# Performance work log

Measured on AMD Instinct MI355X. Metric: run time of the kernel, lower is better.

## Reference

```python
import jax, jax.numpy as jnp
import numpy as np

N_NODES = 50000
HIDDEN = 64
N_EDGES = 800000
HOPS = (1, 2, 3)


def setup_inputs() -> dict:
    key = jax.random.key(0)
    ks = jax.random.split(key, 16)
    d = HIDDEN
    inp = {
        "x": jax.random.normal(ks[0], (N_NODES, d), dtype=jnp.float32),
        "edge_index": jax.random.randint(ks[1], (2, N_EDGES), 0, N_NODES, dtype=jnp.int64),
    }
    s = 1.0 / np.sqrt(d)
    # per-hop GIN MLP params: Linear(d,d) -> ReLU -> Linear(d,d)
    for i in range(len(HOPS)):
        inp[f"W1_{i}"] = jax.random.uniform(ks[2 + 4 * i], (d, d), jnp.float32, -s, s)
        inp[f"b1_{i}"] = jax.random.uniform(ks[3 + 4 * i], (d,), jnp.float32, -s, s)
        inp[f"W2_{i}"] = jax.random.uniform(ks[4 + 4 * i], (d, d), jnp.float32, -s, s)
        inp[f"b2_{i}"] = jax.random.uniform(ks[5 + 4 * i], (d,), jnp.float32, -s, s)
    so = 1.0 / np.sqrt(d * len(HOPS))
    inp["Wo"] = jax.random.uniform(ks[14], (d * len(HOPS), d), jnp.float32, -so, so)
    inp["bo"] = jax.random.uniform(ks[15], (d,), jnp.float32, -so, so)
    return inp


def _gin_conv(h, src, dst, W1, b1, W2, b2):
    # GINConv with eps=0: MLP(x + sum_{j in N(i)} x_j)
    agg = jax.ops.segment_sum(h[src], dst, num_segments=N_NODES)  # [N, d]
    z = h + agg
    z = jax.nn.relu(z @ W1 + b1) @ W2 + b2
    return z


def reference(x, edge_index,
              W1_0, b1_0, W2_0, b2_0,
              W1_1, b1_1, W2_1, b2_1,
              W1_2, b1_2, W2_2, b2_2,
              Wo, bo):
    src, dst = edge_index[0], edge_index[1]
    params = [(W1_0, b1_0, W2_0, b2_0),
              (W1_1, b1_1, W2_1, b2_1),
              (W1_2, b1_2, W2_2, b2_2)]
    outs = []
    for hop, (W1, b1, W2, b2) in zip(HOPS, params):
        h = x
        for _ in range(hop):
            h = _gin_conv(h, src, dst, W1, b1, W2, b2)
        outs.append(h)
    return jnp.concatenate(outs, axis=-1) @ Wo + bo
```

## Files before the change

### kernel.cpp

```cpp
#include <hip/hip_runtime.h>

#define NN 50000
#define NE 800000
#define D  64
#define TILE 64
#define TPB 512
#define NBLK 196


__global__ __launch_bounds__(256) void k_count(const int* __restrict__ ei, int* __restrict__ deg) {
    int e = blockIdx.x * 256 + threadIdx.x;
    if (e < NE) atomicAdd(&deg[ei[NE + e]], 1);
}

__global__ __launch_bounds__(256) void k_bsum(const int* __restrict__ deg, int* __restrict__ bsum) {
    __shared__ int s[256];
    int t = threadIdx.x;
    int i = blockIdx.x * 256 + t;
    s[t] = (i < NN) ? deg[i] : 0;
    __syncthreads();
    for (int off = 128; off > 0; off >>= 1) {
        if (t < off) s[t] += s[t + off];
        __syncthreads();
    }
    if (t == 0) bsum[blockIdx.x] = s[0];
}

__global__ __launch_bounds__(256) void k_scan2(const int* __restrict__ deg,
                                               const int* __restrict__ bsum,
                                               int* __restrict__ row_ptr,
                                               int* __restrict__ cursor) {
    __shared__ int s[256];
    __shared__ int sboff;
    int t = threadIdx.x;
    int b = blockIdx.x;

    int pacc = 0;
    for (int i = t; i < b; i += 256) pacc += bsum[i];
    s[t] = pacc;
    __syncthreads();
    for (int off = 128; off > 0; off >>= 1) {
        if (t < off) s[t] += s[t + off];
        __syncthreads();
    }
    if (t == 0) sboff = s[0];
    __syncthreads();
    int boffv = sboff;
    __syncthreads();

    int i = b * 256 + t;
    int v = (i < NN) ? deg[i] : 0;
    s[t] = v;
    __syncthreads();
    for (int off = 1; off < 256; off <<= 1) {
        int u = (t >= off) ? s[t - off] : 0;
        __syncthreads();
        s[t] += u;
        __syncthreads();
    }
    int excl = s[t] - v + boffv;
    if (i < NN) { row_ptr[i] = excl; cursor[i] = excl; }
    if (b == 0 && t == 0) row_ptr[NN] = NE;
}

__global__ __launch_bounds__(256) void k_fill(const int* __restrict__ ei,
                                              int* __restrict__ cursor,
                                              int* __restrict__ colv) {
    int e = blockIdx.x * 256 + threadIdx.x;
    if (e < NE) {
        int d = ei[NE + e];
        int p = atomicAdd(&cursor[d], 1);
        colv[p] = ei[e];
    }
}


__device__ __forceinline__ float4 gather_row(const float4* __restrict__ h4,
                                             const int* __restrict__ row_ptr,
                                             const int* __restrict__ colv,
                                             int n, int g, int q) {
    float4 a0 = make_float4(0.f, 0.f, 0.f, 0.f);
    float4 a1 = make_float4(0.f, 0.f, 0.f, 0.f);
    float4 a2 = make_float4(0.f, 0.f, 0.f, 0.f);
    float4 a3 = make_float4(0.f, 0.f, 0.f, 0.f);
    if (n >= 0) {
        if (g == 0) a0 = h4[n * 16 + q];
        int e1 = row_ptr[n + 1];
        int e  = row_ptr[n] + g;
        for (; e + 12 < e1; e += 16) {
            int s0 = colv[e], s1 = colv[e + 4], s2 = colv[e + 8], s3 = colv[e + 12];
            float4 v0 = h4[s0 * 16 + q];
            float4 v1 = h4[s1 * 16 + q];
            float4 v2 = h4[s2 * 16 + q];
            float4 v3 = h4[s3 * 16 + q];
            a0.x += v0.x; a0.y += v0.y; a0.z += v0.z; a0.w += v0.w;
            a1.x += v1.x; a1.y += v1.y; a1.z += v1.z; a1.w += v1.w;
            a2.x += v2.x; a2.y += v2.y; a2.z += v2.z; a2.w += v2.w;
            a3.x += v3.x; a3.y += v3.y; a3.z += v3.z; a3.w += v3.w;
        }
        for (; e < e1; e += 4) {
            float4 v = h4[colv[e] * 16 + q];
            a1.x += v.x; a1.y += v.y; a1.z += v.z; a1.w += v.w;
        }
        a0.x += a1.x + a2.x + a3.x;
        a0.y += a1.y + a2.y + a3.y;
        a0.z += a1.z + a2.z + a3.z;
        a0.w += a1.w + a2.w + a3.w;
    }
    a0.x += __shfl_xor(a0.x, 16); a0.y += __shfl_xor(a0.y, 16);
    a0.z += __shfl_xor(a0.z, 16); a0.w += __shfl_xor(a0.w, 16);
    a0.x += __shfl_xor(a0.x, 32); a0.y += __shfl_xor(a0.y, 32);
    a0.z += __shfl_xor(a0.z, 32); a0.w += __shfl_xor(a0.w, 32);
    return a0;
}


__device__ __forceinline__ void conv_body(
    const float4* __restrict__ h4,
    const int* __restrict__ row_ptr,
    const int* __restrict__ colv,
    const float* __restrict__ W1, const float* __restrict__ b1,
    const float* __restrict__ W2, const float* __restrict__ b2,
    float4* __restrict__ out4,
    float (&sW)[D][D], float4 (&sZ4)[TILE][17], float* sB1, float* sB2,
    int node0)
{
    int tid = threadIdx.x;

    {
        const float4* w14 = (const float4*)W1;
        float4* s14 = (float4*)sW;
        for (int i = tid; i < D * D / 4; i += TPB) s14[i] = w14[i];
        if (tid < D) { sB1[tid] = b1[tid]; sB2[tid] = b2[tid]; }
    }

    int wave = tid >> 6, lane = tid & 63;
    int g = lane >> 4, q = lane & 15;

    for (int r = wave; r < TILE; r += (TPB / 64)) {
        int n = node0 + r;
        float4 a = gather_row(h4, row_ptr, colv, (n < NN) ? n : -1, g, q);
        if (g == 0) sZ4[r][q] = a;
    }
    __syncthreads();

    int tr = tid >> 4, tc = tid & 15;
    float* zr0 = (float*)&sZ4[tr * 2 + 0][0];
    float* zr1 = (float*)&sZ4[tr * 2 + 1][0];

    float acc[2][4];
    #pragma unroll
    for (int c = 0; c < 4; ++c) { acc[0][c] = sB1[tc * 4 + c]; acc[1][c] = sB1[tc * 4 + c]; }
    #pragma unroll 16
    for (int k = 0; k < D; ++k) {
        float z0 = zr0[k], z1 = zr1[k];
        #pragma unroll
        for (int c = 0; c < 4; ++c) {
            float w = sW[k][tc * 4 + c];
            acc[0][c] += z0 * w;
            acc[1][c] += z1 * w;
        }
    }
    {
        float4 h0, h1;
        h0.x = fmaxf(acc[0][0], 0.f); h0.y = fmaxf(acc[0][1], 0.f);
        h0.z = fmaxf(acc[0][2], 0.f); h0.w = fmaxf(acc[0][3], 0.f);
        h1.x = fmaxf(acc[1][0], 0.f); h1.y = fmaxf(acc[1][1], 0.f);
        h1.z = fmaxf(acc[1][2], 0.f); h1.w = fmaxf(acc[1][3], 0.f);
        *(float4*)&zr0[tc * 4] = h0;
        *(float4*)&zr1[tc * 4] = h1;
    }
    __syncthreads();

    {
        const float4* w24 = (const float4*)W2;
        float4* s24 = (float4*)sW;
        for (int i = tid; i < D * D / 4; i += TPB) s24[i] = w24[i];
    }
    __syncthreads();

    #pragma unroll
    for (int c = 0; c < 4; ++c) { acc[0][c] = sB2[tc * 4 + c]; acc[1][c] = sB2[tc * 4 + c]; }
    #pragma unroll 16
    for (int k = 0; k < D; ++k) {
        float z0 = zr0[k], z1 = zr1[k];
        #pragma unroll
        for (int c = 0; c < 4; ++c) {
            float w = sW[k][tc * 4 + c];
            acc[0][c] += z0 * w;
            acc[1][c] += z1 * w;
        }
    }
    #pragma unroll
    for (int i = 0; i < 2; ++i) {
        int n = node0 + tr * 2 + i;
        if (n < NN) {
            float4 o;
            o.x = acc[i][0]; o.y = acc[i][1]; o.z = acc[i][2]; o.w = acc[i][3];
            out4[n * 16 + tc] = o;
        }
    }
}

__global__ __launch_bounds__(TPB, 8) void k_conv(
    const float4* __restrict__ h4,
    const int* __restrict__ row_ptr,
    const int* __restrict__ colv,
    const float* __restrict__ W1, const float* __restrict__ b1,
    const float* __restrict__ W2, const float* __restrict__ b2,
    float4* __restrict__ out4)
{
    __shared__ float sW[D][D];
    __shared__ float4 sZ4[TILE][17];
    __shared__ float sB1[D], sB2[D];
    conv_body(h4, row_ptr, colv, W1, b1, W2, b2, out4,
              sW, sZ4, sB1, sB2, blockIdx.x * TILE);
}

__global__ __launch_bounds__(TPB, 8) void k_conv_dual(
    const float4* __restrict__ hA4, const float4* __restrict__ hB4,
    const int* __restrict__ row_ptr,
    const int* __restrict__ colv,
    const float* __restrict__ W1a, const float* __restrict__ b1a,
    const float* __restrict__ W2a, const float* __restrict__ b2a,
    const float* __restrict__ W1b, const float* __restrict__ b1b,
    const float* __restrict__ W2b, const float* __restrict__ b2b,
    float4* __restrict__ outA4, float4* __restrict__ outB4, int nb)
{
    __shared__ float sW[D][D];
    __shared__ float4 sZ4[TILE][17];
    __shared__ float sB1[D], sB2[D];
    int b = blockIdx.x;
    if (b < nb) {
        conv_body(hA4, row_ptr, colv, W1a, b1a, W2a, b2a, outA4,
                  sW, sZ4, sB1, sB2, b * TILE);
    } else {
        conv_body(hB4, row_ptr, colv, W1b, b1b, W2b, b2b, outB4,
                  sW, sZ4, sB1, sB2, (b - nb) * TILE);
    }
}


__global__ __launch_bounds__(TPB) void k_aggmlp3(
    const float4* __restrict__ h4,
    const int* __restrict__ row_ptr,
    const int* __restrict__ colv,
    const float* __restrict__ W1a, const float* __restrict__ b1a,
    const float* __restrict__ W2a, const float* __restrict__ b2a,
    const float* __restrict__ W1b, const float* __restrict__ b1b,
    const float* __restrict__ W2b, const float* __restrict__ b2b,
    const float* __restrict__ W1c, const float* __restrict__ b1c,
    const float* __restrict__ W2c, const float* __restrict__ b2c,
    float4* __restrict__ outA, float4* __restrict__ outB, float4* __restrict__ outC)
{
    __shared__ float sW[D][D];
    __shared__ float4 sZ4[TILE][17];
    __shared__ float4 sH4[TILE][17];
    __shared__ float sB[D];

    int tid = threadIdx.x;
    int node0 = blockIdx.x * TILE;

    int wave = tid >> 6, lane = tid & 63;
    int g = lane >> 4, q = lane & 15;

    for (int r = wave; r < TILE; r += (TPB / 64)) {
        int n = node0 + r;
        float4 a = gather_row(h4, row_ptr, colv, (n < NN) ? n : -1, g, q);
        if (g == 0) sZ4[r][q] = a;
    }

    int tr = tid >> 4, tc = tid & 15;
    float* zr0 = (float*)&sZ4[tr * 2 + 0][0];
    float* zr1 = (float*)&sZ4[tr * 2 + 1][0];
    float* hr0 = (float*)&sH4[tr * 2 + 0][0];
    float* hr1 = (float*)&sH4[tr * 2 + 1][0];

    #pragma unroll 1
    for (int m = 0; m < 3; ++m) {
        const float* W1 = (m == 0) ? W1a : (m == 1) ? W1b : W1c;
        const float* B1 = (m == 0) ? b1a : (m == 1) ? b1b : b1c;
        const float* W2 = (m == 0) ? W2a : (m == 1) ? W2b : W2c;
        const float* B2 = (m == 0) ? b2a : (m == 1) ? b2b : b2c;
        float4* out4 = (m == 0) ? outA : (m == 1) ? outB : outC;

        {
            const float4* w4 = (const float4*)W1;
            float4* s4 = (float4*)sW;
            for (int i = tid; i < D * D / 4; i += TPB) s4[i] = w4[i];
            if (tid < D) sB[tid] = B1[tid];
        }
        __syncthreads();

        float acc[2][4];
        #pragma unroll
        for (int c = 0; c < 4; ++c) { acc[0][c] = sB[tc * 4 + c]; acc[1][c] = sB[tc * 4 + c]; }
        #pragma unroll 16
        for (int k = 0; k < D; ++k) {
            float z0 = zr0[k], z1 = zr1[k];
            #pragma unroll
            for (int c = 0; c < 4; ++c) {
                float w = sW[k][tc * 4 + c];
                acc[0][c] += z0 * w;
                acc[1][c] += z1 * w;
            }
        }
        {
            float4 h0, h1;
            h0.x = fmaxf(acc[0][0], 0.f); h0.y = fmaxf(acc[0][1], 0.f);
            h0.z = fmaxf(acc[0][2], 0.f); h0.w = fmaxf(acc[0][3], 0.f);
            h1.x = fmaxf(acc[1][0], 0.f); h1.y = fmaxf(acc[1][1], 0.f);
            h1.z = fmaxf(acc[1][2], 0.f); h1.w = fmaxf(acc[1][3], 0.f);
            *(float4*)&hr0[tc * 4] = h0;
            *(float4*)&hr1[tc * 4] = h1;
        }
        __syncthreads();

        {
            const float4* w4 = (const float4*)W2;
            float4* s4 = (float4*)sW;
            for (int i = tid; i < D * D / 4; i += TPB) s4[i] = w4[i];
            if (tid < D) sB[tid] = B2[tid];
        }
        __syncthreads();

        #pragma unroll
        for (int c = 0; c < 4; ++c) { acc[0][c] = sB[tc * 4 + c]; acc[1][c] = sB[tc * 4 + c]; }
        #pragma unroll 16
        for (int k = 0; k < D; ++k) {
            float h0 = hr0[k], h1 = hr1[k];
            #pragma unroll
            for (int c = 0; c < 4; ++c) {
                float w = sW[k][tc * 4 + c];
                acc[0][c] += h0 * w;
                acc[1][c] += h1 * w;
            }
        }
        #pragma unroll
        for (int i = 0; i < 2; ++i) {
            int n = node0 + tr * 2 + i;
            if (n < NN) {
                float4 o;
                o.x = acc[i][0]; o.y = acc[i][1]; o.z = acc[i][2]; o.w = acc[i][3];
                out4[n * 16 + tc] = o;
            }
        }
        __syncthreads();
    }
}


__global__ __launch_bounds__(TPB, 8) void k_final(
    const float4* __restrict__ H0, const float4* __restrict__ H1,
    const float4* __restrict__ H2,
    const float* __restrict__ Wo, const float* __restrict__ bo,
    float4* __restrict__ out4)
{
    __shared__ float sW[D][D];
    __shared__ float4 sY4[TILE][17];
    __shared__ float sB[D];

    int tid = threadIdx.x;
    int node0 = blockIdx.x * TILE;
    int tr = tid >> 4, tc = tid & 15;
    const float* yr0 = (const float*)&sY4[tr * 2 + 0][0];
    const float* yr1 = (const float*)&sY4[tr * 2 + 1][0];

    float accO[2][4];

    #pragma unroll 1
    for (int m = 0; m < 3; ++m) {
        const float4* Hc = (m == 0) ? H0 : (m == 1) ? H1 : H2;
        {
            const float4* w4 = (const float4*)(Wo + m * 64 * D);
            float4* s4 = (float4*)sW;
            for (int i = tid; i < D * D / 4; i += TPB) s4[i] = w4[i];
            if (m == 0 && tid < D) sB[tid] = bo[tid];
        }
        for (int i = tid; i < TILE * 16; i += TPB) {
            int r = i >> 4, qq = i & 15;
            int n = node0 + r;
            sY4[r][qq] = (n < NN) ? Hc[n * 16 + qq] : make_float4(0.f, 0.f, 0.f, 0.f);
        }
        __syncthreads();

        if (m == 0) {
            #pragma unroll
            for (int c = 0; c < 4; ++c) { accO[0][c] = sB[tc * 4 + c]; accO[1][c] = sB[tc * 4 + c]; }
        }
        #pragma unroll 16
        for (int k = 0; k < D; ++k) {
            float z0 = yr0[k], z1 = yr1[k];
            #pragma unroll
            for (int c = 0; c < 4; ++c) {
                float w = sW[k][tc * 4 + c];
                accO[0][c] += z0 * w;
                accO[1][c] += z1 * w;
            }
        }
        __syncthreads();
    }

    #pragma unroll
    for (int i = 0; i < 2; ++i) {
        int n = node0 + tr * 2 + i;
        if (n < NN) {
            float4 o;
            o.x = accO[i][0]; o.y = accO[i][1]; o.z = accO[i][2]; o.w = accO[i][3];
            out4[n * 16 + tc] = o;
        }
    }
}


extern "C" void kernel_launch(void* const* d_in, const int* in_sizes, int n_in,
                              void* d_out, int out_size, void* d_ws, size_t ws_size,
                              hipStream_t stream) {
    const float* x    = (const float*)d_in[0];
    const int*   ei   = (const int*)d_in[1];
    const float* W1_0 = (const float*)d_in[2];
    const float* b1_0 = (const float*)d_in[3];
    const float* W2_0 = (const float*)d_in[4];
    const float* b2_0 = (const float*)d_in[5];
    const float* W1_1 = (const float*)d_in[6];
    const float* b1_1 = (const float*)d_in[7];
    const float* W2_1 = (const float*)d_in[8];
    const float* b2_1 = (const float*)d_in[9];
    const float* W1_2 = (const float*)d_in[10];
    const float* b1_2 = (const float*)d_in[11];
    const float* W2_2 = (const float*)d_in[12];
    const float* b2_2 = (const float*)d_in[13];
    const float* Wo   = (const float*)d_in[14];
    const float* bo   = (const float*)d_in[15];
    float4* out = (float4*)d_out;

    char* ws = (char*)d_ws;
    int* deg     = (int*)(ws + 0);
    int* cursor  = (int*)(ws + 200704);
    int* row_ptr = (int*)(ws + 401408);
    int* colv    = (int*)(ws + 602112);
    int* bsum    = (int*)(ws + 3802112);
    float* fbase = (float*)(ws + 3804160);
    float4* H0  = (float4*)(fbase);
    float4* H1  = (float4*)(fbase + 3200000);
    float4* tB  = (float4*)(fbase + 6400000);
    float4* tC2 = (float4*)(fbase + 9600000);
    const float4* x4 = (const float4*)x;

    hipMemsetAsync(deg, 0, NN * sizeof(int), stream);
    k_count<<<(NE + 255) / 256, 256, 0, stream>>>(ei, deg);
    k_bsum <<<NBLK, 256, 0, stream>>>(deg, bsum);
    k_scan2<<<NBLK, 256, 0, stream>>>(deg, bsum, row_ptr, cursor);
    k_fill <<<(NE + 255) / 256, 256, 0, stream>>>(ei, cursor, colv);

    int nb = (NN + TILE - 1) / TILE;

    k_aggmlp3<<<nb, TPB, 0, stream>>>(x4, row_ptr, colv,
                                      W1_0, b1_0, W2_0, b2_0,
                                      W1_1, b1_1, W2_1, b2_1,
                                      W1_2, b1_2, W2_2, b2_2,
                                      H0, tB, out);

    k_conv_dual<<<2 * nb, TPB, 0, stream>>>(
        (const float4*)tB, (const float4*)out, row_ptr, colv,
        W1_1, b1_1, W2_1, b2_1,
        W1_2, b1_2, W2_2, b2_2,
        H1, tC2, nb);

    k_conv<<<nb, TPB, 0, stream>>>((const float4*)tC2, row_ptr, colv,
                                   W1_2, b1_2, W2_2, b2_2, tB);

    k_final<<<nb, TPB, 0, stream>>>((const float4*)H0, (const float4*)H1, (const float4*)tB,
                                    Wo, bo, out);
}
```

Before: 342.6 us.

## Fuse last GIN conv with output projection and drop block-sum scan kernel

```diff
diff --git a/kernel.cpp b/kernel.cpp
--- a/kernel.cpp
+++ b/kernel.cpp
@@ -13,21 +13,7 @@
     if (e < NE) atomicAdd(&deg[ei[NE + e]], 1);
 }
 
-__global__ __launch_bounds__(256) void k_bsum(const int* __restrict__ deg, int* __restrict__ bsum) {
-    __shared__ int s[256];
-    int t = threadIdx.x;
-    int i = blockIdx.x * 256 + t;
-    s[t] = (i < NN) ? deg[i] : 0;
-    __syncthreads();
-    for (int off = 128; off > 0; off >>= 1) {
-        if (t < off) s[t] += s[t + off];
-        __syncthreads();
-    }
-    if (t == 0) bsum[blockIdx.x] = s[0];
-}
-
 __global__ __launch_bounds__(256) void k_scan2(const int* __restrict__ deg,
-                                               const int* __restrict__ bsum,
                                                int* __restrict__ row_ptr,
                                                int* __restrict__ cursor) {
     __shared__ int s[256];
@@ -35,8 +21,9 @@
     int t = threadIdx.x;
     int b = blockIdx.x;
 
+    int lim = b * 256;
     int pacc = 0;
-    for (int i = t; i < b; i += 256) pacc += bsum[i];
+    for (int i = t; i < lim; i += 256) pacc += deg[i];
     s[t] = pacc;
     __syncthreads();
     for (int off = 128; off > 0; off >>= 1) {
@@ -48,7 +35,7 @@
     int boffv = sboff;
     __syncthreads();
 
-    int i = b * 256 + t;
+    int i = lim + t;
     int v = (i < NN) ? deg[i] : 0;
     s[t] = v;
     __syncthreads();
@@ -202,21 +189,6 @@
     }
 }
 
-__global__ __launch_bounds__(TPB, 8) void k_conv(
-    const float4* __restrict__ h4,
-    const int* __restrict__ row_ptr,
-    const int* __restrict__ colv,
-    const float* __restrict__ W1, const float* __restrict__ b1,
-    const float* __restrict__ W2, const float* __restrict__ b2,
-    float4* __restrict__ out4)
-{
-    __shared__ float sW[D][D];
-    __shared__ float4 sZ4[TILE][17];
-    __shared__ float sB1[D], sB2[D];
-    conv_body(h4, row_ptr, colv, W1, b1, W2, b2, out4,
-              sW, sZ4, sB1, sB2, blockIdx.x * TILE);
-}
-
 __global__ __launch_bounds__(TPB, 8) void k_conv_dual(
     const float4* __restrict__ hA4, const float4* __restrict__ hB4,
     const int* __restrict__ row_ptr,
@@ -241,6 +213,161 @@
 }
 
 
+__global__ __launch_bounds__(TPB, 8) void k_conv_last(
+    const float4* __restrict__ h4,
+    const float4* __restrict__ H0, const float4* __restrict__ H1,
+    const int* __restrict__ row_ptr, const int* __restrict__ colv,
+    const float* __restrict__ W1, const float* __restrict__ b1,
+    const float* __restrict__ W2, const float* __restrict__ b2,
+    const float* __restrict__ Wo, const float* __restrict__ bo,
+    float4* __restrict__ out4)
+{
+    __shared__ float sW[D][D];
+    __shared__ float4 sZ4[TILE][17];
+    __shared__ float sB1[D], sB2[D];
+
+    int tid = threadIdx.x;
+    int node0 = blockIdx.x * TILE;
+
+    {
+        const float4* w14 = (const float4*)W1;
+        float4* s14 = (float4*)sW;
+        for (int i = tid; i < D * D / 4; i += TPB) s14[i] = w14[i];
+        if (tid < D) { sB1[tid] = b1[tid]; sB2[tid] = b2[tid]; }
+    }
+
+    int wave = tid >> 6, lane = tid & 63;
+    int g = lane >> 4, q = lane & 15;
+
+    for (int r = wave; r < TILE; r += (TPB / 64)) {
+        int n = node0 + r;
+        float4 a = gather_row(h4, row_ptr, colv, (n < NN) ? n : -1, g, q);
+        if (g == 0) sZ4[r][q] = a;
+    }
+    __syncthreads();
+
+    int tr = tid >> 4, tc = tid & 15;
+    float* zr0 = (float*)&sZ4[tr * 2 + 0][0];
+    float* zr1 = (float*)&sZ4[tr * 2 + 1][0];
+
+    float acc[2][4];
+    #pragma unroll
+    for (int c = 0; c < 4; ++c) { acc[0][c] = sB1[tc * 4 + c]; acc[1][c] = sB1[tc * 4 + c]; }
+    #pragma unroll 16
+    for (int k = 0; k < D; ++k) {
+        float z0 = zr0[k], z1 = zr1[k];
+        #pragma unroll
+        for (int c = 0; c < 4; ++c) {
+            float w = sW[k][tc * 4 + c];
+            acc[0][c] += z0 * w;
+            acc[1][c] += z1 * w;
+        }
+    }
+    {
+        float4 h0, h1;
+        h0.x = fmaxf(acc[0][0], 0.f); h0.y = fmaxf(acc[0][1], 0.f);
+        h0.z = fmaxf(acc[0][2], 0.f); h0.w = fmaxf(acc[0][3], 0.f);
+        h1.x = fmaxf(acc[1][0], 0.f); h1.y = fmaxf(acc[1][1], 0.f);
+        h1.z = fmaxf(acc[1][2], 0.f); h1.w = fmaxf(acc[1][3], 0.f);
+        *(float4*)&zr0[tc * 4] = h0;
+        *(float4*)&zr1[tc * 4] = h1;
+    }
+    __syncthreads();
+
+    {
+        const float4* w24 = (const float4*)W2;
+        float4* s24 = (float4*)sW;
+        for (int i = tid; i < D * D / 4; i += TPB) s24[i] = w24[i];
+    }
+    __syncthreads();
+
+    #pragma unroll
+    for (int c = 0; c < 4; ++c) { acc[0][c] = sB2[tc * 4 + c]; acc[1][c] = sB2[tc * 4 + c]; }
+    #pragma unroll 16
+    for (int k = 0; k < D; ++k) {
+        float z0 = zr0[k], z1 = zr1[k];
+        #pragma unroll
+        for (int c = 0; c < 4; ++c) {
+            float w = sW[k][tc * 4 + c];
+            acc[0][c] += z0 * w;
+            acc[1][c] += z1 * w;
+        }
+    }
+    {
+        float4 h0, h1;
+        h0.x = acc[0][0]; h0.y = acc[0][1]; h0.z = acc[0][2]; h0.w = acc[0][3];
+        h1.x = acc[1][0]; h1.y = acc[1][1]; h1.z = acc[1][2]; h1.w = acc[1][3];
+        *(float4*)&zr0[tc * 4] = h0;
+        *(float4*)&zr1[tc * 4] = h1;
+    }
+    __syncthreads();
+
+    float accO[2][4];
+    int n0 = node0 + tr * 2 + 0;
+    int n1 = node0 + tr * 2 + 1;
+
+    #pragma unroll 1
+    for (int m = 0; m < 3; ++m) {
+        {
+            const float4* w4 = (const float4*)(Wo + m * 64 * D);
+            float4* s4 = (float4*)sW;
+            for (int i = tid; i < D * D / 4; i += TPB) s4[i] = w4[i];
+        }
+        __syncthreads();
+
+        if (m == 0) {
+            #pragma unroll
+            for (int c = 0; c < 4; ++c) { accO[0][c] = sB1[0] * 0.f; }
+            #pragma unroll
+            for (int c = 0; c < 4; ++c) { accO[0][c] = bo[tc * 4 + c]; accO[1][c] = accO[0][c]; }
+        }
+
+        if (m < 2) {
+            const float4* Hc = (m == 0) ? H0 : H1;
+            #pragma unroll 4
+            for (int k4 = 0; k4 < 16; ++k4) {
+                float4 z0v = Hc[n0 * 16 + k4];
+                float4 z1v = Hc[n1 * 16 + k4];
+                #pragma unroll
+                for (int j = 0; j < 4; ++j) {
+                    int k = k4 * 4 + j;
+                    float z0 = (j == 0) ? z0v.x : (j == 1) ? z0v.y : (j == 2) ? z0v.z : z0v.w;
+                    float z1 = (j == 0) ? z1v.x : (j == 1) ? z1v.y : (j == 2) ? z1v.z : z1v.w;
+                    #pragma unroll
+                    for (int c = 0; c < 4; ++c) {
+                        float w = sW[k][tc * 4 + c];
+                        accO[0][c] += z0 * w;
+                        accO[1][c] += z1 * w;
+                    }
+                }
+            }
+        } else {
+            #pragma unroll 16
+            for (int k = 0; k < D; ++k) {
+                float z0 = zr0[k], z1 = zr1[k];
+                #pragma unroll
+                for (int c = 0; c < 4; ++c) {
+                    float w = sW[k][tc * 4 + c];
+                    accO[0][c] += z0 * w;
+                    accO[1][c] += z1 * w;
+                }
+            }
+        }
+        if (m < 2) __syncthreads();
+    }
+
+    #pragma unroll
+    for (int i = 0; i < 2; ++i) {
+        int n = node0 + tr * 2 + i;
+        if (n < NN) {
+            float4 o;
+            o.x = accO[i][0]; o.y = accO[i][1]; o.z = accO[i][2]; o.w = accO[i][3];
+            out4[n * 16 + tc] = o;
+        }
+    }
+}
+
+
 __global__ __launch_bounds__(TPB) void k_aggmlp3(
     const float4* __restrict__ h4,
     const int* __restrict__ row_ptr,
@@ -346,69 +473,6 @@
             }
         }
         __syncthreads();
-    }
-}
-
-
-__global__ __launch_bounds__(TPB, 8) void k_final(
-    const float4* __restrict__ H0, const float4* __restrict__ H1,
-    const float4* __restrict__ H2,
-    const float* __restrict__ Wo, const float* __restrict__ bo,
-    float4* __restrict__ out4)
-{
-    __shared__ float sW[D][D];
-    __shared__ float4 sY4[TILE][17];
-    __shared__ float sB[D];
-
-    int tid = threadIdx.x;
-    int node0 = blockIdx.x * TILE;
-    int tr = tid >> 4, tc = tid & 15;
-    const float* yr0 = (const float*)&sY4[tr * 2 + 0][0];
-    const float* yr1 = (const float*)&sY4[tr * 2 + 1][0];
-
-    float accO[2][4];
-
-    #pragma unroll 1
-    for (int m = 0; m < 3; ++m) {
-        const float4* Hc = (m == 0) ? H0 : (m == 1) ? H1 : H2;
-        {
-            const float4* w4 = (const float4*)(Wo + m * 64 * D);
-            float4* s4 = (float4*)sW;
-            for (int i = tid; i < D * D / 4; i += TPB) s4[i] = w4[i];
-            if (m == 0 && tid < D) sB[tid] = bo[tid];
-        }
-        for (int i = tid; i < TILE * 16; i += TPB) {
-            int r = i >> 4, qq = i & 15;
-            int n = node0 + r;
-            sY4[r][qq] = (n < NN) ? Hc[n * 16 + qq] : make_float4(0.f, 0.f, 0.f, 0.f);
-        }
-        __syncthreads();
-
-        if (m == 0) {
-            #pragma unroll
-            for (int c = 0; c < 4; ++c) { accO[0][c] = sB[tc * 4 + c]; accO[1][c] = sB[tc * 4 + c]; }
-        }
-        #pragma unroll 16
-        for (int k = 0; k < D; ++k) {
-            float z0 = yr0[k], z1 = yr1[k];
-            #pragma unroll
-            for (int c = 0; c < 4; ++c) {
-                float w = sW[k][tc * 4 + c];
-                accO[0][c] += z0 * w;
-                accO[1][c] += z1 * w;
-            }
-        }
-        __syncthreads();
-    }
-
-    #pragma unroll
-    for (int i = 0; i < 2; ++i) {
-        int n = node0 + tr * 2 + i;
-        if (n < NN) {
-            float4 o;
-            o.x = accO[i][0]; o.y = accO[i][1]; o.z = accO[i][2]; o.w = accO[i][3];
-            out4[n * 16 + tc] = o;
-        }
     }
 }
 
@@ -439,7 +503,6 @@
     int* cursor  = (int*)(ws + 200704);
     int* row_ptr = (int*)(ws + 401408);
     int* colv    = (int*)(ws + 602112);
-    int* bsum    = (int*)(ws + 3802112);
     float* fbase = (float*)(ws + 3804160);
     float4* H0  = (float4*)(fbase);
     float4* H1  = (float4*)(fbase + 3200000);
@@ -449,8 +512,7 @@
 
     hipMemsetAsync(deg, 0, NN * sizeof(int), stream);
     k_count<<<(NE + 255) / 256, 256, 0, stream>>>(ei, deg);
-    k_bsum <<<NBLK, 256, 0, stream>>>(deg, bsum);
-    k_scan2<<<NBLK, 256, 0, stream>>>(deg, bsum, row_ptr, cursor);
+    k_scan2<<<NBLK, 256, 0, stream>>>(deg, row_ptr, cursor);
     k_fill <<<(NE + 255) / 256, 256, 0, stream>>>(ei, cursor, colv);
 
     int nb = (NN + TILE - 1) / TILE;
@@ -467,9 +529,9 @@
         W1_2, b1_2, W2_2, b2_2,
         H1, tC2, nb);
 
-    k_conv<<<nb, TPB, 0, stream>>>((const float4*)tC2, row_ptr, colv,
-                                   W1_2, b1_2, W2_2, b2_2, tB);
-
-    k_final<<<nb, TPB, 0, stream>>>((const float4*)H0, (const float4*)H1, (const float4*)tB,
-                                    Wo, bo, out);
-}
+    k_conv_last<<<nb, TPB, 0, stream>>>((const float4*)tC2,
+                                        (const float4*)H0, (const float4*)H1,
+                                        row_ptr, colv,
+                                        W1_2, b1_2, W2_2, b2_2,
+                                        Wo, bo, out);
+}
```

Result: slower. 371.4 us (+8.4%).

## Split first-hop aggregation from the three MLPs and drop the separate block-sum pass

Applied to the files above, without the earlier changes.

```diff
diff --git a/kernel.cpp b/kernel.cpp
--- a/kernel.cpp
+++ b/kernel.cpp
@@ -13,21 +13,7 @@
     if (e < NE) atomicAdd(&deg[ei[NE + e]], 1);
 }
 
-__global__ __launch_bounds__(256) void k_bsum(const int* __restrict__ deg, int* __restrict__ bsum) {
-    __shared__ int s[256];
-    int t = threadIdx.x;
-    int i = blockIdx.x * 256 + t;
-    s[t] = (i < NN) ? deg[i] : 0;
-    __syncthreads();
-    for (int off = 128; off > 0; off >>= 1) {
-        if (t < off) s[t] += s[t + off];
-        __syncthreads();
-    }
-    if (t == 0) bsum[blockIdx.x] = s[0];
-}
-
 __global__ __launch_bounds__(256) void k_scan2(const int* __restrict__ deg,
-                                               const int* __restrict__ bsum,
                                                int* __restrict__ row_ptr,
                                                int* __restrict__ cursor) {
     __shared__ int s[256];
@@ -35,8 +21,9 @@
     int t = threadIdx.x;
     int b = blockIdx.x;
 
+    int lim = b * 256;
     int pacc = 0;
-    for (int i = t; i < b; i += 256) pacc += bsum[i];
+    for (int i = t; i < lim; i += 256) pacc += deg[i];
     s[t] = pacc;
     __syncthreads();
     for (int off = 128; off > 0; off >>= 1) {
@@ -48,7 +35,7 @@
     int boffv = sboff;
     __syncthreads();
 
-    int i = b * 256 + t;
+    int i = lim + t;
     int v = (i < NN) ? deg[i] : 0;
     s[t] = v;
     __syncthreads();
@@ -115,6 +102,124 @@
 }
 
 
+__global__ __launch_bounds__(TPB, 8) void k_gather(
+    const float4* __restrict__ h4,
+    const int* __restrict__ row_ptr,
+    const int* __restrict__ colv,
+    float4* __restrict__ z4)
+{
+    int tid = threadIdx.x;
+    int node0 = blockIdx.x * TILE;
+    int wave = tid >> 6, lane = tid & 63;
+    int g = lane >> 4, q = lane & 15;
+
+    for (int r = wave; r < TILE; r += (TPB / 64)) {
+        int n = node0 + r;
+        float4 a = gather_row(h4, row_ptr, colv, (n < NN) ? n : -1, g, q);
+        if (g == 0 && n < NN) z4[n * 16 + q] = a;
+    }
+}
+
+
+__global__ __launch_bounds__(TPB, 8) void k_mlp3(
+    const float4* __restrict__ z4,
+    const float* __restrict__ W1a, const float* __restrict__ b1a,
+    const float* __restrict__ W2a, const float* __restrict__ b2a,
+    const float* __restrict__ W1b, const float* __restrict__ b1b,
+    const float* __restrict__ W2b, const float* __restrict__ b2b,
+    const float* __restrict__ W1c, const float* __restrict__ b1c,
+    const float* __restrict__ W2c, const float* __restrict__ b2c,
+    float4* __restrict__ outA, float4* __restrict__ outB, float4* __restrict__ outC,
+    int nb)
+{
+    __shared__ float sW[D][D];
+    __shared__ float4 sZ4[TILE][17];
+    __shared__ float sB1[D], sB2[D];
+
+    int b = blockIdx.x;
+    int m = (b < nb) ? 0 : (b < 2 * nb) ? 1 : 2;
+    int node0 = (b - m * nb) * TILE;
+
+    const float* W1 = (m == 0) ? W1a : (m == 1) ? W1b : W1c;
+    const float* B1 = (m == 0) ? b1a : (m == 1) ? b1b : b1c;
+    const float* W2 = (m == 0) ? W2a : (m == 1) ? W2b : W2c;
+    const float* B2 = (m == 0) ? b2a : (m == 1) ? b2b : b2c;
+    float4* out4    = (m == 0) ? outA : (m == 1) ? outB : outC;
+
+    int tid = threadIdx.x;
+
+    {
+        const float4* w14 = (const float4*)W1;
+        float4* s14 = (float4*)sW;
+        for (int i = tid; i < D * D / 4; i += TPB) s14[i] = w14[i];
+        if (tid < D) { sB1[tid] = B1[tid]; sB2[tid] = B2[tid]; }
+    }
+    for (int i = tid; i < TILE * 16; i += TPB) {
+        int r = i >> 4, qq = i & 15;
+        int n = node0 + r;
+        sZ4[r][qq] = (n < NN) ? z4[n * 16 + qq] : make_float4(0.f, 0.f, 0.f, 0.f);
+    }
+    __syncthreads();
+
+    int tr = tid >> 4, tc = tid & 15;
+    float* zr0 = (float*)&sZ4[tr * 2 + 0][0];
+    float* zr1 = (float*)&sZ4[tr * 2 + 1][0];
+
+    float acc[2][4];
+    #pragma unroll
+    for (int c = 0; c < 4; ++c) { acc[0][c] = sB1[tc * 4 + c]; acc[1][c] = sB1[tc * 4 + c]; }
+    #pragma unroll 16
+    for (int k = 0; k < D; ++k) {
+        float z0 = zr0[k], z1 = zr1[k];
+        #pragma unroll
+        for (int c = 0; c < 4; ++c) {
+            float w = sW[k][tc * 4 + c];
+            acc[0][c] += z0 * w;
+            acc[1][c] += z1 * w;
+        }
+    }
+    {
+        float4 h0, h1;
+        h0.x = fmaxf(acc[0][0], 0.f); h0.y = fmaxf(acc[0][1], 0.f);
+        h0.z = fmaxf(acc[0][2], 0.f); h0.w = fmaxf(acc[0][3], 0.f);
+        h1.x = fmaxf(acc[1][0], 0.f); h1.y = fmaxf(acc[1][1], 0.f);
+        h1.z = fmaxf(acc[1][2], 0.f); h1.w = fmaxf(acc[1][3], 0.f);
+        *(float4*)&zr0[tc * 4] = h0;
+        *(float4*)&zr1[tc * 4] = h1;
+    }
+    __syncthreads();
+
+    {
+        const float4* w24 = (const float4*)W2;
+        float4* s24 = (float4*)sW;
+        for (int i = tid; i < D * D / 4; i += TPB) s24[i] = w24[i];
+    }
+    __syncthreads();
+
+    #pragma unroll
+    for (int c = 0; c < 4; ++c) { acc[0][c] = sB2[tc * 4 + c]; acc[1][c] = sB2[tc * 4 + c]; }
+    #pragma unroll 16
+    for (int k = 0; k < D; ++k) {
+        float z0 = zr0[k], z1 = zr1[k];
+        #pragma unroll
+        for (int c = 0; c < 4; ++c) {
+            float w = sW[k][tc * 4 + c];
+            acc[0][c] += z0 * w;
+            acc[1][c] += z1 * w;
+        }
+    }
+    #pragma unroll
+    for (int i = 0; i < 2; ++i) {
+        int n = node0 + tr * 2 + i;
+        if (n < NN) {
+            float4 o;
+            o.x = acc[i][0]; o.y = acc[i][1]; o.z = acc[i][2]; o.w = acc[i][3];
+            out4[n * 16 + tc] = o;
+        }
+    }
+}
+
+
 __device__ __forceinline__ void conv_body(
     const float4* __restrict__ h4,
     const int* __restrict__ row_ptr,
@@ -237,115 +342,6 @@
     } else {
         conv_body(hB4, row_ptr, colv, W1b, b1b, W2b, b2b, outB4,
                   sW, sZ4, sB1, sB2, (b - nb) * TILE);
-    }
-}
-
-
-__global__ __launch_bounds__(TPB) void k_aggmlp3(
-    const float4* __restrict__ h4,
-    const int* __restrict__ row_ptr,
-    const int* __restrict__ colv,
-    const float* __restrict__ W1a, const float* __restrict__ b1a,
-    const float* __restrict__ W2a, const float* __restrict__ b2a,
-    const float* __restrict__ W1b, const float* __restrict__ b1b,
-    const float* __restrict__ W2b, const float* __restrict__ b2b,
-    const float* __restrict__ W1c, const float* __restrict__ b1c,
-    const float* __restrict__ W2c, const float* __restrict__ b2c,
-    float4* __restrict__ outA, float4* __restrict__ outB, float4* __restrict__ outC)
-{
-    __shared__ float sW[D][D];
-    __shared__ float4 sZ4[TILE][17];
-    __shared__ float4 sH4[TILE][17];
-    __shared__ float sB[D];
-
-    int tid = threadIdx.x;
-    int node0 = blockIdx.x * TILE;
-
-    int wave = tid >> 6, lane = tid & 63;
-    int g = lane >> 4, q = lane & 15;
-
-    for (int r = wave; r < TILE; r += (TPB / 64)) {
-        int n = node0 + r;
-        float4 a = gather_row(h4, row_ptr, colv, (n < NN) ? n : -1, g, q);
-        if (g == 0) sZ4[r][q] = a;
-    }
-
-    int tr = tid >> 4, tc = tid & 15;
-    float* zr0 = (float*)&sZ4[tr * 2 + 0][0];
-    float* zr1 = (float*)&sZ4[tr * 2 + 1][0];
-    float* hr0 = (float*)&sH4[tr * 2 + 0][0];
-    float* hr1 = (float*)&sH4[tr * 2 + 1][0];
-
-    #pragma unroll 1
-    for (int m = 0; m < 3; ++m) {
-        const float* W1 = (m == 0) ? W1a : (m == 1) ? W1b : W1c;
-        const float* B1 = (m == 0) ? b1a : (m == 1) ? b1b : b1c;
-        const float* W2 = (m == 0) ? W2a : (m == 1) ? W2b : W2c;
-        const float* B2 = (m == 0) ? b2a : (m == 1) ? b2b : b2c;
-        float4* out4 = (m == 0) ? outA : (m == 1) ? outB : outC;
-
-        {
-            const float4* w4 = (const float4*)W1;
-            float4* s4 = (float4*)sW;
-            for (int i = tid; i < D * D / 4; i += TPB) s4[i] = w4[i];
-            if (tid < D) sB[tid] = B1[tid];
-        }
-        __syncthreads();
-
-        float acc[2][4];
-        #pragma unroll
-        for (int c = 0; c < 4; ++c) { acc[0][c] = sB[tc * 4 + c]; acc[1][c] = sB[tc * 4 + c]; }
-        #pragma unroll 16
-        for (int k = 0; k < D; ++k) {
-            float z0 = zr0[k], z1 = zr1[k];
-            #pragma unroll
-            for (int c = 0; c < 4; ++c) {
-                float w = sW[k][tc * 4 + c];
-                acc[0][c] += z0 * w;
-                acc[1][c] += z1 * w;
-            }
-        }
-        {
-            float4 h0, h1;
-            h0.x = fmaxf(acc[0][0], 0.f); h0.y = fmaxf(acc[0][1], 0.f);
-            h0.z = fmaxf(acc[0][2], 0.f); h0.w = fmaxf(acc[0][3], 0.f);
-            h1.x = fmaxf(acc[1][0], 0.f); h1.y = fmaxf(acc[1][1], 0.f);
-            h1.z = fmaxf(acc[1][2], 0.f); h1.w = fmaxf(acc[1][3], 0.f);
-            *(float4*)&hr0[tc * 4] = h0;
-            *(float4*)&hr1[tc * 4] = h1;
-        }
-        __syncthreads();
-
-        {
-            const float4* w4 = (const float4*)W2;
-            float4* s4 = (float4*)sW;
-            for (int i = tid; i < D * D / 4; i += TPB) s4[i] = w4[i];
-            if (tid < D) sB[tid] = B2[tid];
-        }
-        __syncthreads();
-
-        #pragma unroll
-        for (int c = 0; c < 4; ++c) { acc[0][c] = sB[tc * 4 + c]; acc[1][c] = sB[tc * 4 + c]; }
-        #pragma unroll 16
-        for (int k = 0; k < D; ++k) {
-            float h0 = hr0[k], h1 = hr1[k];
-            #pragma unroll
-            for (int c = 0; c < 4; ++c) {
-                float w = sW[k][tc * 4 + c];
-                acc[0][c] += h0 * w;
-                acc[1][c] += h1 * w;
-            }
-        }
-        #pragma unroll
-        for (int i = 0; i < 2; ++i) {
-            int n = node0 + tr * 2 + i;
-            if (n < NN) {
-                float4 o;
-                o.x = acc[i][0]; o.y = acc[i][1]; o.z = acc[i][2]; o.w = acc[i][3];
-                out4[n * 16 + tc] = o;
-            }
-        }
-        __syncthreads();
     }
 }
 
@@ -439,7 +435,6 @@
     int* cursor  = (int*)(ws + 200704);
     int* row_ptr = (int*)(ws + 401408);
     int* colv    = (int*)(ws + 602112);
-    int* bsum    = (int*)(ws + 3802112);
     float* fbase = (float*)(ws + 3804160);
     float4* H0  = (float4*)(fbase);
     float4* H1  = (float4*)(fbase + 3200000);
@@ -449,17 +444,18 @@
 
     hipMemsetAsync(deg, 0, NN * sizeof(int), stream);
     k_count<<<(NE + 255) / 256, 256, 0, stream>>>(ei, deg);
-    k_bsum <<<NBLK, 256, 0, stream>>>(deg, bsum);
-    k_scan2<<<NBLK, 256, 0, stream>>>(deg, bsum, row_ptr, cursor);
+    k_scan2<<<NBLK, 256, 0, stream>>>(deg, row_ptr, cursor);
     k_fill <<<(NE + 255) / 256, 256, 0, stream>>>(ei, cursor, colv);
 
     int nb = (NN + TILE - 1) / TILE;
 
-    k_aggmlp3<<<nb, TPB, 0, stream>>>(x4, row_ptr, colv,
-                                      W1_0, b1_0, W2_0, b2_0,
-                                      W1_1, b1_1, W2_1, b2_1,
-                                      W1_2, b1_2, W2_2, b2_2,
-                                      H0, tB, out);
+    k_gather<<<nb, TPB, 0, stream>>>(x4, row_ptr, colv, tC2);
+
+    k_mlp3<<<3 * nb, TPB, 0, stream>>>((const float4*)tC2,
+                                       W1_0, b1_0, W2_0, b2_0,
+                                       W1_1, b1_1, W2_1, b2_1,
+                                       W1_2, b1_2, W2_2, b2_2,
+                                       H0, tB, out, nb);
 
     k_conv_dual<<<2 * nb, TPB, 0, stream>>>(
         (const float4*)tB, (const float4*)out, row_ptr, colv,
```

Result: no change. 348.4 us (+1.7%).
